# Performance work log

Hardware: AMD Instinct MI355X
Metric: run time of the kernel (lower is better)

The kernel has to match this reference:

```python
import jax, jax.numpy as jnp
import numpy as np

B, S, E, H, FFN, NQ, DEPTH = 2, 2048, 1024, 16, 4096, 4, 2
DK = E // H
LN_EPS = 1e-5


def _layernorm(t, g, b):
    m = t.mean(-1, keepdims=True)
    v = ((t - m) ** 2).mean(-1, keepdims=True)
    return (t - m) / jnp.sqrt(v + LN_EPS) * g + b


def setup_inputs() -> dict:
    key = jax.random.key(0)
    ks = jax.random.split(key, 12)
    n = lambda i, shape, sc=1.0: (jax.random.normal(ks[i], shape, jnp.float32) * sc)
    return {
        "x": n(0, (B, S, E)),
        "wq": n(1, (E, E), 0.02),
        "wk": n(2, (E, E), 0.02),
        "wv": n(3, (E, E), 0.02),
        "wo": n(4, (E, E), 0.02),
        "w1": n(5, (E, FFN), 0.02),
        "b1": jnp.zeros((FFN,), jnp.float32),
        "w2": n(6, (FFN, E), 0.02),
        "b2": jnp.zeros((E,), jnp.float32),
        "qp_attn": n(7, (NQ, DEPTH)),
        "qp_ffn": n(8, (NQ, DEPTH)),
        "ln1_g": jnp.ones((E,), jnp.float32),
        "ln1_b": jnp.zeros((E,), jnp.float32),
        "ln2_g": jnp.ones((E,), jnp.float32),
        "ln2_b": jnp.zeros((E,), jnp.float32),
    }


def reference(x, wq, wk, wv, wo, w1, b1, w2, b2, qp_attn, qp_ffn,
              ln1_g, ln1_b, ln2_g, ln2_b):
    b, s, _ = x.shape
    # --- quantum attention ---
    q = (x @ wq).reshape(b, s, H, DK)
    k = (x @ wk).reshape(b, s, H, DK)
    v = (x @ wv).reshape(b, s, H, DK)
    scores = jnp.einsum('bqhd,bkhd->bhqk', q, k) / np.sqrt(DK).astype(np.float32)
    attn = jax.nn.softmax(scores, axis=-1)
    classical = jnp.einsum('bhqk,bkhd->bqhd', attn, v)  # (b, s, H, DK)
    # depth-2 RX-only circuit on |0..0>: <Z_0> = cos(sum_d params[0, d]);
    # data-independent scalar broadcast to the first NQ channels of each head
    c_attn = jnp.cos(qp_attn[0].sum())
    mixed = classical.at[..., :NQ].add(c_attn)
    attn_out = mixed.reshape(b, s, E) @ wo
    x1 = _layernorm(x + attn_out, ln1_g, ln1_b)  # dropout is identity in eval
    # --- quantum feed-forward ---
    h = x1 @ w1 + b1  # computed in the source but never consumed by the circuit
    # depth-2 RY-only circuit: <Z_0> = cos(sum_d params[0, d]) -- also data-free
    c_ffn = jnp.cos(qp_ffn[0].sum())
    qvec = jnp.zeros((FFN,), x.dtype).at[:NQ].set(c_ffn)
    ffn_out = jax.nn.relu(qvec) @ w2 + b2  # (E,), broadcast per token
    return _layernorm(x1 + ffn_out, ln2_g, ln2_b)
```

## Files before the change

### kernel.cpp

```cpp
#include <hip/hip_runtime.h>
#include <hip/hip_bf16.h>

typedef unsigned short u16;
using short8 = __attribute__((ext_vector_type(8))) short;
using f32x4  = __attribute__((ext_vector_type(4))) float;
using u32x2  = __attribute__((ext_vector_type(2))) unsigned;

#define S_  2048
#define E_  1024
#define H_  16
#define DK_ 64

#define GLP(p)  ((const __attribute__((address_space(1))) void*)(p))
#define LDSP(p) ((__attribute__((address_space(3))) void*)(p))

__device__ __forceinline__ float b2f(u16 u) {
  union { unsigned int i; float f; } v; v.i = ((unsigned int)u) << 16; return v.f;
}
__device__ __forceinline__ u16 f2b(float f) {
  union { float f; unsigned int i; } v; v.f = f;
  unsigned int r = v.i + 0x7fffu + ((v.i >> 16) & 1u);
  return (u16)(r >> 16);
}
__device__ __forceinline__ unsigned pk2(float a, float b) {
  __hip_bfloat162 h = __float22bfloat162_rn(make_float2(a, b));
  union { __hip_bfloat162 h; unsigned u; } c; c.h = h; return c.u;
}
__device__ __forceinline__ float fexp2(float x) {
#if __has_builtin(__builtin_amdgcn_exp2f)
  return __builtin_amdgcn_exp2f(x);
#else
  return exp2f(x);
#endif
}
__device__ __forceinline__ void plane32_swap(unsigned &dst, unsigned &src) {
#if __has_builtin(__builtin_amdgcn_permlane32_swap)
  u32x2 r = __builtin_amdgcn_permlane32_swap(dst, src, false, false);
  dst = r[0]; src = r[1];
#else
  asm volatile("v_permlane32_swap_b32 %0, %1" : "+v"(dst), "+v"(src));
#endif
}
__device__ __forceinline__ void plane16_swap(unsigned &dst, unsigned &src) {
#if __has_builtin(__builtin_amdgcn_permlane16_swap)
  u32x2 r = __builtin_amdgcn_permlane16_swap(dst, src, false, false);
  dst = r[0]; src = r[1];
#else
  asm volatile("v_permlane16_swap_b32 %0, %1" : "+v"(dst), "+v"(src));
#endif
}

__global__ __launch_bounds__(256) void prep_k(
    const float* __restrict__ x,
    const float* __restrict__ wq, const float* __restrict__ wk,
    const float* __restrict__ wv, const float* __restrict__ wo,
    const float* __restrict__ w2, const float* __restrict__ b2,
    const float* __restrict__ qpf,
    u16* __restrict__ xb, u16* __restrict__ wt, float* __restrict__ fv) {
  __shared__ u16 tile[64][65];
  int id = blockIdx.x, t = threadIdx.x;
  if (id < 2048) {
    size_t i = ((size_t)id * 256 + t) * 8;
    float4 a = *(const float4*)&x[i];
    float4 b = *(const float4*)&x[i + 4];
    uint4 o;
    o.x = pk2(a.x, a.y); o.y = pk2(a.z, a.w);
    o.z = pk2(b.x, b.y); o.w = pk2(b.z, b.w);
    *(uint4*)&xb[i] = o;
  } else if (id < 3072) {
    int i = id - 2048;
    int z = i >> 8; i &= 255;
    const float* src = (z == 0) ? wq : (z == 1) ? wk : (z == 2) ? wv : wo;
    u16* dst = wt + (size_t)z * E_ * E_;
    int k0 = (i & 15) * 64, n0 = (i >> 4) * 64;
    int rr = t >> 4, c4 = (t & 15) * 4;
    for (int p = 0; p < 4; p++) {
      int r = p * 16 + rr;
      float4 v = *(const float4*)&src[(size_t)(k0 + r) * E_ + n0 + c4];
      tile[r][c4] = f2b(v.x); tile[r][c4 + 1] = f2b(v.y);
      tile[r][c4 + 2] = f2b(v.z); tile[r][c4 + 3] = f2b(v.w);
    }
    __syncthreads();
    for (int p = 0; p < 4; p++) {
      int r = p * 16 + rr;
      ushort4 o;
      o.x = tile[c4][r]; o.y = tile[c4 + 1][r]; o.z = tile[c4 + 2][r]; o.w = tile[c4 + 3][r];
      *(ushort4*)&dst[(size_t)(n0 + r) * E_ + k0 + c4] = o;
    }
  } else {
    int e = (id - 3072) * 256 + t;
    float r = fmaxf(cosf(qpf[0] + qpf[1]), 0.f);
    fv[e] = b2[e] + r * (w2[0 * E_ + e] + w2[1 * E_ + e] + w2[2 * E_ + e] + w2[3 * E_ + e]);
  }
}

__device__ __forceinline__ void gemm_loop97(
    const u16* __restrict__ A, const u16* __restrict__ Bt,
    int m0, int n0, f32x4 acc[4][4], u16 (*As)[128][32], u16 (*Bs)[128][32]) {
  int t = threadIdx.x, lane = t & 63, w = t >> 6;
  int wm = w >> 1, wn = w & 1, l15 = lane & 15, quad = lane >> 4;
  int srow = lane >> 2, sch = (lane & 3) * 8;
  const u16 *ga[2], *gb[2];
#pragma unroll
  for (int p = 0; p < 2; p++) {
    int seg = w * 2 + p;
    ga[p] = A + (size_t)(m0 + seg * 16 + srow) * E_ + sch;
    gb[p] = Bt + (size_t)(n0 + seg * 16 + srow) * E_ + sch;
  }
#pragma unroll
  for (int p = 0; p < 2; p++) {
    int seg = w * 2 + p;
    __builtin_amdgcn_global_load_lds(GLP(ga[p]), LDSP(&As[0][seg * 16][0]), 16, 0, 0);
    __builtin_amdgcn_global_load_lds(GLP(gb[p]), LDSP(&Bs[0][seg * 16][0]), 16, 0, 0);
    ga[p] += 32; gb[p] += 32;
  }
  for (int i = 0; i < 32; i++) {
    __syncthreads();
    if (i + 1 < 32) {
      int nb = (i + 1) & 1;
#pragma unroll
      for (int p = 0; p < 2; p++) {
        int seg = w * 2 + p;
        __builtin_amdgcn_global_load_lds(GLP(ga[p]), LDSP(&As[nb][seg * 16][0]), 16, 0, 0);
        __builtin_amdgcn_global_load_lds(GLP(gb[p]), LDSP(&Bs[nb][seg * 16][0]), 16, 0, 0);
        ga[p] += 32; gb[p] += 32;
      }
    }
    int cb = i & 1;
    short8 af[4], bf[4];
#pragma unroll
    for (int ii = 0; ii < 4; ii++) af[ii] = *(const short8*)&As[cb][wm * 64 + ii * 16 + l15][quad * 8];
#pragma unroll
    for (int j = 0; j < 4; j++) bf[j] = *(const short8*)&Bs[cb][wn * 64 + j * 16 + l15][quad * 8];
#pragma unroll
    for (int ii = 0; ii < 4; ii++)
#pragma unroll
      for (int j = 0; j < 4; j++)
        acc[ii][j] = __builtin_amdgcn_mfma_f32_16x16x32_bf16(af[ii], bf[j], acc[ii][j], 0, 0, 0);
  }
}

__global__ __launch_bounds__(256) void qkv_gemm(
    const u16* __restrict__ xb, const u16* __restrict__ wt,
    u16* __restrict__ q, u16* __restrict__ k, u16* __restrict__ vt) {
  __shared__ __align__(16) u16 As[2][128][32];
  __shared__ __align__(16) u16 Bs[2][128][32];
  int n0 = blockIdx.x * 128, m0 = blockIdx.y * 128, z = blockIdx.z;
  const u16* Bt = wt + (size_t)z * E_ * E_;
  f32x4 acc[4][4];
  f32x4 zero = {0.f, 0.f, 0.f, 0.f};
  for (int i = 0; i < 4; i++)
    for (int j = 0; j < 4; j++) acc[i][j] = zero;
  gemm_loop97(xb, Bt, m0, n0, acc, As, Bs);
  int t = threadIdx.x, lane = t & 63, w = t >> 6;
  int wm = w >> 1, wn = w & 1, l15 = lane & 15, quad = lane >> 4;
  if (z < 2) {
    u16* out = (z == 0) ? q : k;
    float sc = (z == 0) ? 0.18033688f : 1.f;
#pragma unroll
    for (int i = 0; i < 4; i++)
#pragma unroll
      for (int j = 0; j < 4; j++) {
        int mm = m0 + wm * 64 + i * 16 + quad * 4;
        int nn = n0 + wn * 64 + j * 16 + l15;
#pragma unroll
        for (int rr = 0; rr < 4; rr++)
          out[(size_t)(mm + rr) * E_ + nn] = f2b(acc[i][j][rr] * sc);
      }
  } else {
#pragma unroll
    for (int i = 0; i < 4; i++)
#pragma unroll
      for (int j = 0; j < 4; j++) {
        int mm = m0 + wm * 64 + i * 16 + quad * 4;
        int nn = n0 + wn * 64 + j * 16 + l15;
        int b = mm >> 11, s = mm & (S_ - 1);
        size_t base = ((size_t)(b * H_ + (nn >> 6)) * DK_ + (nn & 63)) * S_ + s;
        ushort4 pk;
        pk.x = f2b(acc[i][j][0]); pk.y = f2b(acc[i][j][1]);
        pk.z = f2b(acc[i][j][2]); pk.w = f2b(acc[i][j][3]);
        *(ushort4*)&vt[base] = pk;
      }
  }
}

__global__ __launch_bounds__(256) void oproj_gemm(
    const u16* __restrict__ am, const u16* __restrict__ wot, float* __restrict__ proj) {
  __shared__ __align__(16) u16 As[2][128][32];
  __shared__ __align__(16) u16 Bs[2][128][32];
  int n0 = blockIdx.x * 128, m0 = blockIdx.y * 128;
  f32x4 acc[4][4];
  f32x4 zero = {0.f, 0.f, 0.f, 0.f};
  for (int i = 0; i < 4; i++)
    for (int j = 0; j < 4; j++) acc[i][j] = zero;
  gemm_loop97(am, wot, m0, n0, acc, As, Bs);
  int t = threadIdx.x, lane = t & 63, w = t >> 6;
  int wm = w >> 1, wn = w & 1, l15 = lane & 15, quad = lane >> 4;
#pragma unroll
  for (int i = 0; i < 4; i++)
#pragma unroll
    for (int j = 0; j < 4; j++) {
      int mm = m0 + wm * 64 + i * 16 + quad * 4;
      int nn = n0 + wn * 64 + j * 16 + l15;
#pragma unroll
      for (int rr = 0; rr < 4; rr++)
        proj[(size_t)(mm + rr) * E_ + nn] = acc[i][j][rr];
    }
}

__global__ __launch_bounds__(256, 4) void attn_kernel(
    const u16* __restrict__ q, const u16* __restrict__ kk,
    const u16* __restrict__ vt, const float* __restrict__ qpa,
    u16* __restrict__ outm) {
  __shared__ __align__(16) u16 Ks[2][64][64];
  __shared__ __align__(16) u16 Vts[2][64][64];
  int bid = blockIdx.x + blockIdx.y * 32;
  int swz = (bid & 7) * 128 + (bid >> 3);
  int qt = swz & 31, bh = swz >> 5;
  int b = bh >> 4, h = bh & 15;
  int q0 = qt * 64;
  int t = threadIdx.x, lane = t & 63, w = t >> 6;
  int l15 = lane & 15, quad = lane >> 4;
  float c_attn = cosf(qpa[0] + qpa[1]);
  int r8 = lane >> 3, slot = lane & 7;
  size_t kbase = (size_t)(b * S_) * E_ + h * DK_;
  size_t vbase = (size_t)(b * H_ + h) * DK_ * S_;
  const u16 *kptr[2], *vptr[2];
#pragma unroll
  for (int p = 0; p < 2; p++) {
    int row = w * 16 + p * 8 + r8;
    int c = slot ^ (row & 7);
    kptr[p] = kk + kbase + (size_t)row * E_ + c * 8;
    vptr[p] = vt + vbase + (size_t)row * S_ + c * 8;
    __builtin_amdgcn_global_load_lds(GLP(kptr[p]), LDSP(&Ks[0][w * 16 + p * 8][0]), 16, 0, 0);
    __builtin_amdgcn_global_load_lds(GLP(vptr[p]), LDSP(&Vts[0][w * 16 + p * 8][0]), 16, 0, 0);
    kptr[p] += (size_t)64 * E_;
    vptr[p] += 64;
  }
  short8 bq[2];
  {
    const u16* gq = q + (size_t)(b * S_ + q0 + w * 16 + l15) * E_ + h * DK_ + quad * 8;
    bq[0] = *(const short8*)gq;
    bq[1] = *(const short8*)(gq + 32);
  }
  short8 bones;
#pragma unroll
  for (int i = 0; i < 8; i++) bones[i] = (short)0x3F80;
  f32x4 O[4], Osum;
  f32x4 zero = {0.f, 0.f, 0.f, 0.f};
  Osum = zero;
#pragma unroll
  for (int j = 0; j < 4; j++) O[j] = zero;
  __syncthreads();
  for (int kt = 0; kt < S_ / 64; kt++) {
    if (kt) __syncthreads();
    if (kt + 1 < S_ / 64) {
      int nb2 = (kt + 1) & 1;
#pragma unroll
      for (int p = 0; p < 2; p++) {
        __builtin_amdgcn_global_load_lds(GLP(kptr[p]), LDSP(&Ks[nb2][w * 16 + p * 8][0]), 16, 0, 0);
        __builtin_amdgcn_global_load_lds(GLP(vptr[p]), LDSP(&Vts[nb2][w * 16 + p * 8][0]), 16, 0, 0);
        kptr[p] += (size_t)64 * E_;
        vptr[p] += 64;
      }
    }
    int cb = kt & 1;
    f32x4 sc[4];
    __builtin_amdgcn_s_setprio(1);
#pragma unroll
    for (int mb = 0; mb < 4; mb++) {
      int row = mb * 16 + l15;
      int c0 = quad ^ (row & 7);
      short8 a0 = *(const short8*)&Ks[cb][row][c0 * 8];
      short8 a1 = *(const short8*)&Ks[cb][row][(c0 ^ 4) * 8];
      f32x4 z = __builtin_amdgcn_mfma_f32_16x16x32_bf16(a0, bq[0], zero, 0, 0, 0);
      sc[mb] = __builtin_amdgcn_mfma_f32_16x16x32_bf16(a1, bq[1], z, 0, 0, 0);
    }
    __builtin_amdgcn_s_setprio(0);
    short8 bv[4][2];
#pragma unroll
    for (int nd = 0; nd < 4; nd++) {
      int rv = nd * 16 + l15;
      int cv = quad ^ (rv & 7);
      bv[nd][0] = *(const short8*)&Vts[cb][rv][cv * 8];
      bv[nd][1] = *(const short8*)&Vts[cb][rv][(cv ^ 4) * 8];
    }
    unsigned W[4][2];
#pragma unroll
    for (int mb = 0; mb < 4; mb++) {
      float p0 = fexp2(sc[mb][0]);
      float p1 = fexp2(sc[mb][1]);
      float p2 = fexp2(sc[mb][2]);
      float p3 = fexp2(sc[mb][3]);
      W[mb][0] = pk2(p0, p1);
      W[mb][1] = pk2(p2, p3);
    }
    union AP { unsigned u[4]; short8 s; };
    AP ap0, ap1;
#pragma unroll
    for (int hh = 0; hh < 2; hh++) {
      {
        unsigned a = W[0][hh], b = W[1][hh];
        plane32_swap(b, a);
        plane16_swap(a, b);
        ap0.u[hh] = a; ap0.u[2 + hh] = b;
      }
      {
        unsigned a = W[2][hh], b = W[3][hh];
        plane32_swap(b, a);
        plane16_swap(a, b);
        ap1.u[hh] = a; ap1.u[2 + hh] = b;
      }
    }
    __builtin_amdgcn_s_setprio(1);
#pragma unroll
    for (int nd = 0; nd < 4; nd++) {
      O[nd] = __builtin_amdgcn_mfma_f32_16x16x32_bf16(ap0.s, bv[nd][0], O[nd], 0, 0, 0);
      O[nd] = __builtin_amdgcn_mfma_f32_16x16x32_bf16(ap1.s, bv[nd][1], O[nd], 0, 0, 0);
    }
    Osum = __builtin_amdgcn_mfma_f32_16x16x32_bf16(ap0.s, bones, Osum, 0, 0, 0);
    Osum = __builtin_amdgcn_mfma_f32_16x16x32_bf16(ap1.s, bones, Osum, 0, 0, 0);
    __builtin_amdgcn_s_setprio(0);
  }
  float inv[4];
#pragma unroll
  for (int r = 0; r < 4; r++) inv[r] = 1.f / Osum[r];
#pragma unroll
  for (int nd = 0; nd < 4; nd++)
#pragma unroll
    for (int r = 0; r < 4; r++) {
      float val = O[nd][r] * inv[r];
      int d = nd * 16 + l15;
      if (nd == 0 && l15 < 4) val += c_attn;
      int tok = b * S_ + q0 + w * 16 + quad * 4 + r;
      outm[(size_t)tok * E_ + h * DK_ + d] = f2b(val);
    }
}

__global__ __launch_bounds__(256) void ln_fused(
    const float* __restrict__ x, const float* __restrict__ proj, const float* __restrict__ fv,
    const float* __restrict__ g1, const float* __restrict__ bb1,
    const float* __restrict__ g2, const float* __restrict__ bb2,
    float* __restrict__ out) {
  __shared__ float sm[8];
  int tok = blockIdx.x, t = threadIdx.x;
  int e0 = t * 4;
  float4 xv = *(const float4*)&x[(size_t)tok * E_ + e0];
  float4 pv = *(const float4*)&proj[(size_t)tok * E_ + e0];
  float v0 = xv.x + pv.x, v1 = xv.y + pv.y;
  float v2 = xv.z + pv.z, v3 = xv.w + pv.w;
  float s = v0 + v1 + v2 + v3;
  float sq = v0 * v0 + v1 * v1 + v2 * v2 + v3 * v3;
  for (int m = 32; m >= 1; m >>= 1) { s += __shfl_xor(s, m, 64); sq += __shfl_xor(sq, m, 64); }
  int wid = t >> 6, lane = t & 63;
  if (lane == 0) { sm[wid] = s; sm[4 + wid] = sq; }
  __syncthreads();
  s = sm[0] + sm[1] + sm[2] + sm[3];
  sq = sm[4] + sm[5] + sm[6] + sm[7];
  float mean = s * (1.f / E_);
  float var = sq * (1.f / E_) - mean * mean;
  float rstd = rsqrtf(var + 1e-5f);
  float4 g1v = *(const float4*)&g1[e0];
  float4 b1v = *(const float4*)&bb1[e0];
  float4 fvv = *(const float4*)&fv[e0];
  float t0 = (v0 - mean) * rstd * g1v.x + b1v.x + fvv.x;
  float t1 = (v1 - mean) * rstd * g1v.y + b1v.y + fvv.y;
  float t2 = (v2 - mean) * rstd * g1v.z + b1v.z + fvv.z;
  float t3 = (v3 - mean) * rstd * g1v.w + b1v.w + fvv.w;
  float s2 = t0 + t1 + t2 + t3;
  float sq2 = t0 * t0 + t1 * t1 + t2 * t2 + t3 * t3;
  for (int m = 32; m >= 1; m >>= 1) { s2 += __shfl_xor(s2, m, 64); sq2 += __shfl_xor(sq2, m, 64); }
  __syncthreads();
  if (lane == 0) { sm[wid] = s2; sm[4 + wid] = sq2; }
  __syncthreads();
  s2 = sm[0] + sm[1] + sm[2] + sm[3];
  sq2 = sm[4] + sm[5] + sm[6] + sm[7];
  float mean2 = s2 * (1.f / E_);
  float var2 = sq2 * (1.f / E_) - mean2 * mean2;
  float rstd2 = rsqrtf(var2 + 1e-5f);
  float4 g2v = *(const float4*)&g2[e0];
  float4 b2v = *(const float4*)&bb2[e0];
  float4 ov;
  ov.x = (t0 - mean2) * rstd2 * g2v.x + b2v.x;
  ov.y = (t1 - mean2) * rstd2 * g2v.y + b2v.y;
  ov.z = (t2 - mean2) * rstd2 * g2v.z + b2v.z;
  ov.w = (t3 - mean2) * rstd2 * g2v.w + b2v.w;
  *(float4*)&out[(size_t)tok * E_ + e0] = ov;
}

extern "C" void kernel_launch(void* const* d_in, const int* in_sizes, int n_in,
                              void* d_out, int out_size, void* d_ws, size_t ws_size,
                              hipStream_t stream) {
  const float* x   = (const float*)d_in[0];
  const float* wq  = (const float*)d_in[1];
  const float* wk  = (const float*)d_in[2];
  const float* wv  = (const float*)d_in[3];
  const float* wo  = (const float*)d_in[4];
  const float* w2  = (const float*)d_in[7];
  const float* b2  = (const float*)d_in[8];
  const float* qpa = (const float*)d_in[9];
  const float* qpf = (const float*)d_in[10];
  const float* g1  = (const float*)d_in[11];
  const float* bb1 = (const float*)d_in[12];
  const float* g2  = (const float*)d_in[13];
  const float* bb2 = (const float*)d_in[14];

  char* ws = (char*)d_ws;
  u16* wt     = (u16*)ws;
  u16* q      = (u16*)(ws + (size_t)8  * 1048576);
  u16* k      = (u16*)(ws + (size_t)16 * 1048576);
  float* proj = (float*)(ws + (size_t)8 * 1048576);
  float* fv   = (float*)(ws + (size_t)24 * 1048576);
  u16* xb     = (u16*)d_out;
  u16* am     = (u16*)d_out;
  u16* vt     = (u16*)d_out + (size_t)4 * 1048576;
  float* outp = (float*)d_out;

  prep_k<<<dim3(3076), 256, 0, stream>>>(x, wq, wk, wv, wo, w2, b2, qpf, xb, wt, fv);
  qkv_gemm<<<dim3(8, 32, 3), 256, 0, stream>>>(xb, wt, q, k, vt);
  attn_kernel<<<dim3(32, 32), 256, 0, stream>>>(q, k, vt, qpa, am);
  oproj_gemm<<<dim3(8, 32), 256, 0, stream>>>(am, wt + (size_t)3 * E_ * E_, proj);
  ln_fused<<<dim3(4096), 256, 0, stream>>>(x, proj, fv, g1, bb1, g2, bb2, outp);
}
```

Before: 247.5 us.

## Split attention work 2x2 across waves by query and key halves with LDS reduction

The attention kernel now assigns each wave 32 queries and half of each 64-key tile instead of 16 queries over all 64 keys. Each K fragment loaded from LDS is reused across two query blocks and each wave reads half the V fragments, which cuts LDS read traffic per MFMA. The two key-half partial outputs and row sums are combined through LDS at the end, adding a reduction step, an extra barrier and more accumulator registers.

```diff
diff --git a/kernel.cpp b/kernel.cpp
--- a/kernel.cpp
+++ b/kernel.cpp
@@ -212,8 +212,7 @@
     const u16* __restrict__ q, const u16* __restrict__ kk,
     const u16* __restrict__ vt, const float* __restrict__ qpa,
     u16* __restrict__ outm) {
-  __shared__ __align__(16) u16 Ks[2][64][64];
-  __shared__ __align__(16) u16 Vts[2][64][64];
+  __shared__ __align__(16) u16 KV[2][2][64][64];
   int bid = blockIdx.x + blockIdx.y * 32;
   int swz = (bid & 7) * 128 + (bid >> 3);
   int qt = swz & 31, bh = swz >> 5;
@@ -221,6 +220,7 @@
   int q0 = qt * 64;
   int t = threadIdx.x, lane = t & 63, w = t >> 6;
   int l15 = lane & 15, quad = lane >> 4;
+  int qh = w >> 1, kh = w & 1;
   float c_attn = cosf(qpa[0] + qpa[1]);
   int r8 = lane >> 3, slot = lane & 7;
   size_t kbase = (size_t)(b * S_) * E_ + h * DK_;
@@ -232,25 +232,29 @@
     int c = slot ^ (row & 7);
     kptr[p] = kk + kbase + (size_t)row * E_ + c * 8;
     vptr[p] = vt + vbase + (size_t)row * S_ + c * 8;
-    __builtin_amdgcn_global_load_lds(GLP(kptr[p]), LDSP(&Ks[0][w * 16 + p * 8][0]), 16, 0, 0);
-    __builtin_amdgcn_global_load_lds(GLP(vptr[p]), LDSP(&Vts[0][w * 16 + p * 8][0]), 16, 0, 0);
+    __builtin_amdgcn_global_load_lds(GLP(kptr[p]), LDSP(&KV[0][0][w * 16 + p * 8][0]), 16, 0, 0);
+    __builtin_amdgcn_global_load_lds(GLP(vptr[p]), LDSP(&KV[0][1][w * 16 + p * 8][0]), 16, 0, 0);
     kptr[p] += (size_t)64 * E_;
     vptr[p] += 64;
   }
-  short8 bq[2];
-  {
-    const u16* gq = q + (size_t)(b * S_ + q0 + w * 16 + l15) * E_ + h * DK_ + quad * 8;
-    bq[0] = *(const short8*)gq;
-    bq[1] = *(const short8*)(gq + 32);
+  short8 bq[2][2];
+#pragma unroll
+  for (int nb = 0; nb < 2; nb++) {
+    const u16* gq = q + (size_t)(b * S_ + q0 + qh * 32 + nb * 16 + l15) * E_ + h * DK_ + quad * 8;
+    bq[nb][0] = *(const short8*)gq;
+    bq[nb][1] = *(const short8*)(gq + 32);
   }
   short8 bones;
 #pragma unroll
   for (int i = 0; i < 8; i++) bones[i] = (short)0x3F80;
-  f32x4 O[4], Osum;
+  f32x4 O[2][4], Osum[2];
   f32x4 zero = {0.f, 0.f, 0.f, 0.f};
-  Osum = zero;
-#pragma unroll
-  for (int j = 0; j < 4; j++) O[j] = zero;
+#pragma unroll
+  for (int nb = 0; nb < 2; nb++) {
+    Osum[nb] = zero;
+#pragma unroll
+    for (int j = 0; j < 4; j++) O[nb][j] = zero;
+  }
   __syncthreads();
   for (int kt = 0; kt < S_ / 64; kt++) {
     if (kt) __syncthreads();
@@ -258,83 +262,112 @@
       int nb2 = (kt + 1) & 1;
 #pragma unroll
       for (int p = 0; p < 2; p++) {
-        __builtin_amdgcn_global_load_lds(GLP(kptr[p]), LDSP(&Ks[nb2][w * 16 + p * 8][0]), 16, 0, 0);
-        __builtin_amdgcn_global_load_lds(GLP(vptr[p]), LDSP(&Vts[nb2][w * 16 + p * 8][0]), 16, 0, 0);
+        __builtin_amdgcn_global_load_lds(GLP(kptr[p]), LDSP(&KV[nb2][0][w * 16 + p * 8][0]), 16, 0, 0);
+        __builtin_amdgcn_global_load_lds(GLP(vptr[p]), LDSP(&KV[nb2][1][w * 16 + p * 8][0]), 16, 0, 0);
         kptr[p] += (size_t)64 * E_;
         vptr[p] += 64;
       }
     }
     int cb = kt & 1;
-    f32x4 sc[4];
+    f32x4 sc[2][2];
     __builtin_amdgcn_s_setprio(1);
 #pragma unroll
-    for (int mb = 0; mb < 4; mb++) {
-      int row = mb * 16 + l15;
+    for (int mb = 0; mb < 2; mb++) {
+      int row = kh * 32 + mb * 16 + l15;
       int c0 = quad ^ (row & 7);
-      short8 a0 = *(const short8*)&Ks[cb][row][c0 * 8];
-      short8 a1 = *(const short8*)&Ks[cb][row][(c0 ^ 4) * 8];
-      f32x4 z = __builtin_amdgcn_mfma_f32_16x16x32_bf16(a0, bq[0], zero, 0, 0, 0);
-      sc[mb] = __builtin_amdgcn_mfma_f32_16x16x32_bf16(a1, bq[1], z, 0, 0, 0);
+      short8 a0 = *(const short8*)&KV[cb][0][row][c0 * 8];
+      short8 a1 = *(const short8*)&KV[cb][0][row][(c0 ^ 4) * 8];
+#pragma unroll
+      for (int nb = 0; nb < 2; nb++) {
+        f32x4 z = __builtin_amdgcn_mfma_f32_16x16x32_bf16(a0, bq[nb][0], zero, 0, 0, 0);
+        sc[mb][nb] = __builtin_amdgcn_mfma_f32_16x16x32_bf16(a1, bq[nb][1], z, 0, 0, 0);
+      }
     }
     __builtin_amdgcn_s_setprio(0);
-    short8 bv[4][2];
+    short8 bv[4];
 #pragma unroll
     for (int nd = 0; nd < 4; nd++) {
       int rv = nd * 16 + l15;
-      int cv = quad ^ (rv & 7);
-      bv[nd][0] = *(const short8*)&Vts[cb][rv][cv * 8];
-      bv[nd][1] = *(const short8*)&Vts[cb][rv][(cv ^ 4) * 8];
-    }
-    unsigned W[4][2];
-#pragma unroll
-    for (int mb = 0; mb < 4; mb++) {
-      float p0 = fexp2(sc[mb][0]);
-      float p1 = fexp2(sc[mb][1]);
-      float p2 = fexp2(sc[mb][2]);
-      float p3 = fexp2(sc[mb][3]);
-      W[mb][0] = pk2(p0, p1);
-      W[mb][1] = pk2(p2, p3);
-    }
+      int cv = (quad | (kh << 2)) ^ (rv & 7);
+      bv[nd] = *(const short8*)&KV[cb][1][rv][cv * 8];
+    }
+    unsigned W[2][2][2];
+#pragma unroll
+    for (int mb = 0; mb < 2; mb++)
+#pragma unroll
+      for (int nb = 0; nb < 2; nb++) {
+        float p0 = fexp2(sc[mb][nb][0]);
+        float p1 = fexp2(sc[mb][nb][1]);
+        float p2 = fexp2(sc[mb][nb][2]);
+        float p3 = fexp2(sc[mb][nb][3]);
+        W[mb][nb][0] = pk2(p0, p1);
+        W[mb][nb][1] = pk2(p2, p3);
+      }
     union AP { unsigned u[4]; short8 s; };
-    AP ap0, ap1;
-#pragma unroll
-    for (int hh = 0; hh < 2; hh++) {
-      {
-        unsigned a = W[0][hh], b = W[1][hh];
-        plane32_swap(b, a);
-        plane16_swap(a, b);
-        ap0.u[hh] = a; ap0.u[2 + hh] = b;
-      }
-      {
-        unsigned a = W[2][hh], b = W[3][hh];
-        plane32_swap(b, a);
-        plane16_swap(a, b);
-        ap1.u[hh] = a; ap1.u[2 + hh] = b;
-      }
-    }
+    AP ap[2];
+#pragma unroll
+    for (int nb = 0; nb < 2; nb++)
+#pragma unroll
+      for (int hh = 0; hh < 2; hh++) {
+        unsigned a = W[0][nb][hh], bw = W[1][nb][hh];
+        plane32_swap(bw, a);
+        plane16_swap(a, bw);
+        ap[nb].u[hh] = a; ap[nb].u[2 + hh] = bw;
+      }
     __builtin_amdgcn_s_setprio(1);
 #pragma unroll
-    for (int nd = 0; nd < 4; nd++) {
-      O[nd] = __builtin_amdgcn_mfma_f32_16x16x32_bf16(ap0.s, bv[nd][0], O[nd], 0, 0, 0);
-      O[nd] = __builtin_amdgcn_mfma_f32_16x16x32_bf16(ap1.s, bv[nd][1], O[nd], 0, 0, 0);
-    }
-    Osum = __builtin_amdgcn_mfma_f32_16x16x32_bf16(ap0.s, bones, Osum, 0, 0, 0);
-    Osum = __builtin_amdgcn_mfma_f32_16x16x32_bf16(ap1.s, bones, Osum, 0, 0, 0);
+    for (int nb = 0; nb < 2; nb++) {
+#pragma unroll
+      for (int nd = 0; nd < 4; nd++)
+        O[nb][nd] = __builtin_amdgcn_mfma_f32_16x16x32_bf16(ap[nb].s, bv[nd], O[nb][nd], 0, 0, 0);
+      Osum[nb] = __builtin_amdgcn_mfma_f32_16x16x32_bf16(ap[nb].s, bones, Osum[nb], 0, 0, 0);
+    }
     __builtin_amdgcn_s_setprio(0);
   }
-  float inv[4];
-#pragma unroll
-  for (int r = 0; r < 4; r++) inv[r] = 1.f / Osum[r];
-#pragma unroll
-  for (int nd = 0; nd < 4; nd++)
-#pragma unroll
-    for (int r = 0; r < 4; r++) {
-      float val = O[nd][r] * inv[r];
-      int d = nd * 16 + l15;
-      if (nd == 0 && l15 < 4) val += c_attn;
-      int tok = b * S_ + q0 + w * 16 + quad * 4 + r;
-      outm[(size_t)tok * E_ + h * DK_ + d] = f2b(val);
-    }
+  float* red = (float*)KV;
+  __syncthreads();
+  if (kh) {
+    float* dst = red + ((size_t)(qh * 64 + lane)) * 44;
+#pragma unroll
+    for (int nb = 0; nb < 2; nb++) {
+#pragma unroll
+      for (int nd = 0; nd < 4; nd++)
+        *(f32x4*)&dst[nb * 16 + nd * 4] = O[nb][nd];
+      *(f32x4*)&dst[32 + nb * 4] = Osum[nb];
+    }
+  }
+  __syncthreads();
+  if (!kh) {
+    const float* src = red + ((size_t)(qh * 64 + lane)) * 44;
+#pragma unroll
+    for (int nb = 0; nb < 2; nb++) {
+#pragma unroll
+      for (int nd = 0; nd < 4; nd++) {
+        f32x4 o2 = *(const f32x4*)&src[nb * 16 + nd * 4];
+#pragma unroll
+        for (int r = 0; r < 4; r++) O[nb][nd][r] += o2[r];
+      }
+      f32x4 s2 = *(const f32x4*)&src[32 + nb * 4];
+#pragma unroll
+      for (int r = 0; r < 4; r++) Osum[nb][r] += s2[r];
+    }
+#pragma unroll
+    for (int nb = 0; nb < 2; nb++) {
+      float inv[4];
+#pragma unroll
+      for (int r = 0; r < 4; r++) inv[r] = 1.f / Osum[nb][r];
+#pragma unroll
+      for (int nd = 0; nd < 4; nd++)
+#pragma unroll
+        for (int r = 0; r < 4; r++) {
+          float val = O[nb][nd][r] * inv[r];
+          int d = nd * 16 + l15;
+          if (nd == 0 && l15 < 4) val += c_attn;
+          int tok = b * S_ + q0 + qh * 32 + nb * 16 + quad * 4 + r;
+          outm[(size_t)tok * E_ + h * DK_ + d] = f2b(val);
+        }
+    }
+  }
 }
 
 __global__ __launch_bounds__(256) void ln_fused(
```

Measured after the change: 244.2 us. Within noise of the previous version (-1.3%).
